# Kernel optimization log

Measured on AMD Instinct MI355X. Metric: run time of the kernel, lower is better.

The kernel has to match this reference:

```python
import jax, jax.numpy as jnp
import numpy as np

NUM_REP = 3

def setup_inputs() -> dict:
    N, E, DIM, R2, L, B, NEG = 20000, 100000, 32, 100, 4, 4, 32
    ks = jax.random.split(jax.random.key(0), 12)
    # all negatives in a row share the same head (required by the model's assert)
    h = jax.random.randint(ks[0], (B, 1), 0, N)
    t = jax.random.randint(ks[1], (B, NEG), 0, N)
    batch = jnp.stack([jnp.broadcast_to(h, (B, NEG)), t], axis=-1)  # [B,NEG,2]
    edge_index = jax.random.randint(ks[2], (2, E), 0, N)
    edge_type = jax.random.randint(ks[3], (E,), 0, R2)
    edge_attr = 0.1 * jax.random.normal(ks[4], (E, DIM), jnp.float32)
    start_query = jax.random.normal(ks[5], (NUM_REP, DIM), jnp.float32)
    W_rel = jax.random.normal(ks[6], (L, DIM, R2 * DIM), jnp.float32) * (DIM ** -0.5)
    b_rel = jnp.zeros((L, R2 * DIM), jnp.float32)
    W_lin = jax.random.normal(ks[7], (L, 2 * DIM, DIM), jnp.float32) * ((2 * DIM) ** -0.5)
    b_lin = jnp.zeros((L, DIM), jnp.float32)
    W_mlp1 = jax.random.normal(ks[8], (DIM, DIM), jnp.float32) * (DIM ** -0.5)
    b_mlp1 = jnp.zeros((DIM,), jnp.float32)
    W_mlp2 = jax.random.normal(ks[9], (DIM, DIM), jnp.float32) * (DIM ** -0.5)
    b_mlp2 = jnp.zeros((DIM,), jnp.float32)
    return {"batch": batch, "edge_index": edge_index, "edge_type": edge_type,
            "edge_attr": edge_attr, "num_nodes": N, "start_query": start_query,
            "W_rel": W_rel, "b_rel": b_rel, "W_lin": W_lin, "b_lin": b_lin,
            "W_mlp1": W_mlp1, "b_mlp1": b_mlp1, "W_mlp2": W_mlp2, "b_mlp2": b_mlp2}

def reference(batch, edge_index, edge_type, edge_attr, num_nodes, start_query,
              W_rel, b_rel, W_lin, b_lin, W_mlp1, b_mlp1, W_mlp2, b_mlp2):
    B, num_neg, _ = batch.shape
    N = int(num_nodes)
    dim = start_query.shape[1]
    L = W_rel.shape[0]
    bs = NUM_REP * B
    batch_full = jnp.tile(batch, (NUM_REP, 1, 1))            # [bs, neg, 2]
    query_idx = jnp.repeat(jnp.arange(NUM_REP), B)           # [bs]
    h_index, t_index = batch_full[..., 0], batch_full[..., 1]
    # negative_sample_to_tail (no-op when heads are constant per row, as built)
    is_t_neg = jnp.all(h_index == h_index[:, :1], axis=-1, keepdims=True)
    h_index, t_index = (jnp.where(is_t_neg, h_index, t_index),
                        jnp.where(is_t_neg, t_index, h_index))
    h0 = h_index[:, 0]
    q = start_query[query_idx]                               # [bs, dim]
    rows = jnp.arange(bs)
    boundary = jnp.zeros((bs, N, dim), q.dtype).at[rows, h0].add(q)
    pb = jnp.zeros((bs, N), q.dtype).at[rows, h0].set(1.0)   # path boundary
    src, dst = edge_index[0], edge_index[1]
    x = boundary
    for l in range(L):
        # dependent per-query relation embeddings: [bs, 2R, dim]
        rel = (q @ W_rel[l] + b_rel[l]).reshape(bs, -1, dim)
        rel_e = rel[:, edge_type] + edge_attr[None]          # [bs, E, dim]
        msg = x[:, src] * rel_e                              # distmult message
        # sum aggregation; boundary acts as the self-loop message
        agg = jnp.zeros((bs, N, dim), x.dtype).at[:, dst].add(msg) + boundary
        x = jax.nn.relu(jnp.concatenate([x, agg], axis=-1) @ W_lin[l] + b_lin[l])
        # reachability propagation of the path boundary (scatter-max)
        pb = jnp.maximum(pb, jnp.zeros((bs, N), pb.dtype).at[:, dst].max(pb[:, src]))
    feat_t = x[rows[:, None], t_index]                       # [bs, neg, dim]
    feat = feat_t.reshape(NUM_REP, B, num_neg, dim).mean(0)  # mean over reps
    features = jax.nn.relu(feat @ W_mlp1 + b_mlp1) @ W_mlp2 + b_mlp2
    pb_t = pb[rows[:, None], t_index][..., None]             # [bs, neg, 1]
    path_boundary = pb_t.reshape(NUM_REP, B, num_neg, 1).max(0)
    return features, path_boundary
```

## Files before the change

kernel.cpp:

```cpp
#include <hip/hip_runtime.h>

#define N_NODES 20000
#define N_EDGES 100000
#define DIM 32
#define R2 100
#define NLAYERS 4
#define BATCH 4
#define NEG 32
#define NREP 3
#define BS (NREP * BATCH)
#define RELDIM (R2 * DIM)

#define NPB 4
#define TPN 96
#define LBLK (NPB * TPN)
#define GRID_LAYER (N_NODES / NPB)

#define EB ((N_EDGES + 255) / 256)
#define NB ((N_NODES + 255) / 256)
#define RELB ((NLAYERS * R2 * BS * DIM) / 256)
#define PREP_GRID (EB + NB + RELB)

#define XO_A 0
#define XO_B (XO_A + (size_t)N_NODES * BS * DIM)
#define PBO_A (XO_B + (size_t)N_NODES * BS * DIM)
#define PBO_B (PBO_A + (size_t)N_NODES * BS)
#define RELO (PBO_B + (size_t)N_NODES * BS)
#define QO (RELO + (size_t)NLAYERS * R2 * BS * DIM)
#define FLOAT_TOTAL (QO + (size_t)BS * DIM)

#define IO_H0 0
#define IO_TIDX (IO_H0 + BS)
#define IO_COUNTS (IO_TIDX + BS * NEG)
#define IO_OFF (IO_COUNTS + N_NODES)
#define IO_BCUR (IO_OFF + N_NODES + 1)
#define IO_CURSOR (IO_BCUR + 256 * 32)
#define IO_ORDER (IO_CURSOR + N_NODES)
#define IO_PAD (IO_ORDER + N_NODES)
#define IO_ES (((IO_PAD + 1) / 2) * 2)
#define INT_TOTAL (IO_ES + 2 * N_EDGES)

__global__ void k_count(const int* __restrict__ dst, int* __restrict__ counts) {
    int e = blockIdx.x * blockDim.x + threadIdx.x;
    if (e < N_EDGES) atomicAdd(&counts[dst[e]], 1);
}

__global__ void k_scan(const int* __restrict__ counts, int* __restrict__ off,
                       int* __restrict__ cursor, int* __restrict__ bcursor,
                       const int* __restrict__ batch,
                       const float* __restrict__ start_query,
                       float* __restrict__ q, int* __restrict__ h0,
                       int* __restrict__ t_idx) {
    __shared__ int sd[1024];
    __shared__ int hist[256];
    int t = threadIdx.x;

    if (t < BS) {
        int r = t;
        int b = r % BATCH, rep = r / BATCH;
        int h00 = batch[(b * NEG + 0) * 2 + 0];
        bool is_t_neg = true;
        for (int j = 0; j < NEG; j++)
            if (batch[(b * NEG + j) * 2 + 0] != h00) { is_t_neg = false; break; }
        int hsel = is_t_neg ? 0 : 1;
        int h0v = batch[(b * NEG + 0) * 2 + hsel];
        h0[r] = h0v;
        for (int j = 0; j < NEG; j++)
            t_idx[r * NEG + j] = batch[(b * NEG + j) * 2 + (1 - hsel)];
        for (int d = 0; d < DIM; d++) q[r * DIM + d] = start_query[rep * DIM + d];
    }

    const int CH = (N_NODES + 1023) / 1024;
    int base = t * CH;
    for (int i = t; i < 256; i += 1024) hist[i] = 0;
    int sum = 0;
    for (int i = 0; i < CH; i++) {
        int idx = base + i;
        if (idx < N_NODES) sum += counts[idx];
    }
    sd[t] = sum;
    __syncthreads();
    for (int o = 1; o < 1024; o <<= 1) {
        int v = (t >= o) ? sd[t - o] : 0;
        __syncthreads();
        sd[t] += v;
        __syncthreads();
    }
    int excl = sd[t] - sum;
    int run = excl;
    for (int i = 0; i < CH; i++) {
        int idx = base + i;
        if (idx < N_NODES) {
            int c = counts[idx];
            off[idx] = run;
            cursor[idx] = run;
            run += c;
            atomicAdd(&hist[c < 255 ? c : 255], 1);
        }
    }
    if (t == 1023) off[N_NODES] = sd[1023];
    __syncthreads();
    if (t == 0) {
        int acc = 0;
        for (int b = 255; b >= 0; b--) { bcursor[b * 32] = acc; acc += hist[b]; }
    }
}

__global__ void k_prep(const int* __restrict__ src, const int* __restrict__ dst,
                       const int* __restrict__ etype, int* __restrict__ cursor,
                       int2* __restrict__ es,
                       const int* __restrict__ counts, int* __restrict__ bcursor,
                       int* __restrict__ node_order,
                       const float* __restrict__ q, const float* __restrict__ W_rel,
                       const float* __restrict__ b_rel, float* __restrict__ rel) {
    int bid = blockIdx.x;
    if (bid < EB) {
        int e = bid * 256 + threadIdx.x;
        if (e < N_EDGES) {
            int p = atomicAdd(&cursor[dst[e]], 1);
            es[p] = make_int2(src[e] | (etype[e] << 20), e);
        }
    } else if (bid < EB + NB) {
        int n = (bid - EB) * 256 + threadIdx.x;
        if (n < N_NODES) {
            int deg = counts[n]; if (deg > 255) deg = 255;
            int pos = atomicAdd(&bcursor[deg * 32], 1);
            node_order[pos] = n;
        }
    } else {
        int idx = (bid - EB - NB) * 256 + threadIdx.x;
        int d = idx & 31;
        int r = (idx >> 5) % BS;
        int et = (idx / (BS * DIM)) % R2;
        int l = idx / (R2 * BS * DIM);
        int c = et * DIM + d;
        const float* W = W_rel + (size_t)l * DIM * RELDIM;
        float acc = b_rel[l * RELDIM + c];
        #pragma unroll
        for (int k = 0; k < DIM; k++) acc += q[r * DIM + k] * W[(size_t)k * RELDIM + c];
        rel[idx] = acc;
    }
}

template <bool L0>
__launch_bounds__(LBLK)
__global__ void k_layer(const float* __restrict__ x_old, const float* __restrict__ pb_old,
                        const float* __restrict__ rel_l, const float* __restrict__ edge_attr,
                        const int2* __restrict__ es, const int* __restrict__ off,
                        const int* __restrict__ node_order,
                        const int* __restrict__ h0, const float* __restrict__ q,
                        const float* __restrict__ W_lin_l, const float* __restrict__ b_lin_l,
                        float* __restrict__ x_new, float* __restrict__ pb_new) {
    __shared__ float sW[64 * DIM];
    __shared__ float sB[DIM];
    __shared__ float sIn[NPB * BS * 68];
    __shared__ int sFlag;

    const int gi = threadIdx.x / TPN;
    const int t = threadIdx.x % TPN;
    const int r = t >> 3;
    const int l = t & 7;
    const int n = node_order[blockIdx.x * NPB + gi];

    const int h0r = h0[r];
    const float4 q4 = *(const float4*)(q + r * DIM + l * 4);
    const int s0 = off[n], s1 = off[n + 1];

    if (L0) {
        if (threadIdx.x == 0) sFlag = 0;
        bool spec = (n == h0r);
        for (int k = s0; k < s1; k++) {
            int2 p2 = es[k];
            if ((p2.x & 0xFFFFF) == h0r) spec = true;
        }
        __syncthreads();
        if (spec) sFlag = 1;
        __syncthreads();
        if (!sFlag) {
            float4 b4 = *(const float4*)(b_lin_l + l * 4);
            b4.x = fmaxf(b4.x, 0.f); b4.y = fmaxf(b4.y, 0.f);
            b4.z = fmaxf(b4.z, 0.f); b4.w = fmaxf(b4.w, 0.f);
            *(float4*)(x_new + ((size_t)n * BS + r) * DIM + l * 4) = b4;
            if (l == 0) pb_new[n * BS + r] = 0.f;
            return;
        }
    }

    for (int i = threadIdx.x; i < 64 * DIM; i += LBLK) sW[i] = W_lin_l[i];
    if (threadIdx.x < DIM) sB[threadIdx.x] = b_lin_l[threadIdx.x];

    float4 xr4, ag4 = make_float4(0.f, 0.f, 0.f, 0.f);
    float pbm;
    if (L0) {
        xr4 = (n == h0r) ? q4 : make_float4(0.f, 0.f, 0.f, 0.f);
        pbm = (n == h0r) ? 1.f : 0.f;
    } else {
        xr4 = *(const float4*)(x_old + ((size_t)n * BS + r) * DIM + l * 4);
        pbm = pb_old[n * BS + r];
    }

    #pragma unroll 2
    for (int k = s0; k < s1; k++) {
        int2 p2 = es[k];
        int s = p2.x & 0xFFFFF;
        int et = ((unsigned)p2.x) >> 20;
        int e = p2.y;
        if (L0) {
            if (s == h0r) {
                float4 rl = *(const float4*)(rel_l + ((size_t)et * BS + r) * DIM + l * 4);
                float4 ea = *(const float4*)(edge_attr + (size_t)e * DIM + l * 4);
                ag4.x += q4.x * (rl.x + ea.x);
                ag4.y += q4.y * (rl.y + ea.y);
                ag4.z += q4.z * (rl.z + ea.z);
                ag4.w += q4.w * (rl.w + ea.w);
                pbm = 1.f;
            }
        } else {
            float4 xs = *(const float4*)(x_old + ((size_t)s * BS + r) * DIM + l * 4);
            float4 rl = *(const float4*)(rel_l + ((size_t)et * BS + r) * DIM + l * 4);
            float4 ea = *(const float4*)(edge_attr + (size_t)e * DIM + l * 4);
            ag4.x += xs.x * (rl.x + ea.x);
            ag4.y += xs.y * (rl.y + ea.y);
            ag4.z += xs.z * (rl.z + ea.z);
            ag4.w += xs.w * (rl.w + ea.w);
            pbm = fmaxf(pbm, pb_old[s * BS + r]);
        }
    }
    if (n == h0r) {
        ag4.x += q4.x; ag4.y += q4.y; ag4.z += q4.z; ag4.w += q4.w;
    }

    float* srow = sIn + (gi * BS + r) * 68;
    *(float4*)(srow + l * 4) = xr4;
    *(float4*)(srow + 32 + l * 4) = ag4;
    __syncthreads();

    float4 acc = *(const float4*)(sB + l * 4);
    #pragma unroll
    for (int k4 = 0; k4 < 16; k4++) {
        float4 v = *(const float4*)(srow + k4 * 4);
        const float* wb = sW + (k4 * 4) * DIM + l * 4;
        float4 w0 = *(const float4*)(wb);
        float4 w1 = *(const float4*)(wb + DIM);
        float4 w2 = *(const float4*)(wb + 2 * DIM);
        float4 w3 = *(const float4*)(wb + 3 * DIM);
        acc.x += v.x * w0.x + v.y * w1.x + v.z * w2.x + v.w * w3.x;
        acc.y += v.x * w0.y + v.y * w1.y + v.z * w2.y + v.w * w3.y;
        acc.z += v.x * w0.z + v.y * w1.z + v.z * w2.z + v.w * w3.z;
        acc.w += v.x * w0.w + v.y * w1.w + v.z * w2.w + v.w * w3.w;
    }
    acc.x = fmaxf(acc.x, 0.f);
    acc.y = fmaxf(acc.y, 0.f);
    acc.z = fmaxf(acc.z, 0.f);
    acc.w = fmaxf(acc.w, 0.f);
    *(float4*)(x_new + ((size_t)n * BS + r) * DIM + l * 4) = acc;
    if (l == 0) pb_new[n * BS + r] = pbm;
}

__launch_bounds__(1024)
__global__ void k_final(const float* __restrict__ x, const float* __restrict__ pb,
                        const int* __restrict__ t_idx,
                        const float* __restrict__ W1, const float* __restrict__ b1,
                        const float* __restrict__ W2, const float* __restrict__ b2,
                        float* __restrict__ out) {
    __shared__ float sW1[DIM * DIM];
    __shared__ float sW2[DIM * DIM];
    __shared__ float sfeat[BATCH * NEG * DIM];
    __shared__ float shid[BATCH * NEG * DIM];
    const int t = threadIdx.x;
    const int NPAIR = BATCH * NEG;

    for (int i = t; i < DIM * DIM; i += 1024) { sW1[i] = W1[i]; sW2[i] = W2[i]; }

    for (int i = t; i < NPAIR * DIM; i += 1024) {
        int pair = i >> 5;
        int d = i & 31;
        int b = pair >> 5;
        int tt = t_idx[pair];
        float s = 0.f;
        #pragma unroll
        for (int rep = 0; rep < NREP; rep++)
            s += x[((size_t)tt * BS + rep * BATCH + b) * DIM + d];
        sfeat[i] = s * (1.f / 3.f);
    }
    __syncthreads();

    for (int i = t; i < NPAIR * DIM; i += 1024) {
        int pair = i >> 5;
        int jj = i & 31;
        float a = b1[jj];
        #pragma unroll
        for (int k = 0; k < DIM; k++)
            a += sfeat[pair * DIM + k] * sW1[k * DIM + jj];
        shid[i] = fmaxf(a, 0.f);
    }
    __syncthreads();

    for (int i = t; i < NPAIR * DIM; i += 1024) {
        int pair = i >> 5;
        int jj = i & 31;
        float a = b2[jj];
        #pragma unroll
        for (int k = 0; k < DIM; k++)
            a += shid[pair * DIM + k] * sW2[k * DIM + jj];
        out[i] = a;
    }

    if (t < NPAIR) {
        int b = t >> 5;
        int tt = t_idx[t];
        float pm = 0.f;
        #pragma unroll
        for (int rep = 0; rep < NREP; rep++)
            pm = fmaxf(pm, pb[(size_t)tt * BS + rep * BATCH + b]);
        out[NPAIR * DIM + t] = pm;
    }
}

extern "C" void kernel_launch(void* const* d_in, const int* in_sizes, int n_in,
                              void* d_out, int out_size, void* d_ws, size_t ws_size,
                              hipStream_t stream) {
    const int* batch = (const int*)d_in[0];
    const int* edge_index = (const int*)d_in[1];
    const int* edge_type = (const int*)d_in[2];
    const float* edge_attr = (const float*)d_in[3];
    const float* start_query = (const float*)d_in[5];
    const float* W_rel = (const float*)d_in[6];
    const float* b_rel = (const float*)d_in[7];
    const float* W_lin = (const float*)d_in[8];
    const float* b_lin = (const float*)d_in[9];
    const float* W_mlp1 = (const float*)d_in[10];
    const float* b_mlp1 = (const float*)d_in[11];
    const float* W_mlp2 = (const float*)d_in[12];
    const float* b_mlp2 = (const float*)d_in[13];

    float* wf = (float*)d_ws;
    int* wi = (int*)(wf + FLOAT_TOTAL);
    size_t need = FLOAT_TOTAL * sizeof(float) + INT_TOTAL * sizeof(int);
    if (ws_size < need) return;

    float* x_a = wf + XO_A;
    float* x_b = wf + XO_B;
    float* pb_a = wf + PBO_A;
    float* pb_b = wf + PBO_B;
    float* rel = wf + RELO;
    float* q = wf + QO;
    int* h0 = wi + IO_H0;
    int* t_idx = wi + IO_TIDX;
    int* counts = wi + IO_COUNTS;
    int* off = wi + IO_OFF;
    int* bcursor = wi + IO_BCUR;
    int* cursor = wi + IO_CURSOR;
    int* node_order = wi + IO_ORDER;
    int2* es = (int2*)(wi + IO_ES);

    const int* src = edge_index;
    const int* dst = edge_index + N_EDGES;

    hipMemsetAsync(counts, 0, (size_t)N_NODES * sizeof(int), stream);

    k_count<<<EB, 256, 0, stream>>>(dst, counts);
    k_scan<<<1, 1024, 0, stream>>>(counts, off, cursor, bcursor,
                                   batch, start_query, q, h0, t_idx);
    k_prep<<<PREP_GRID, 256, 0, stream>>>(src, dst, edge_type, cursor, es,
                                          counts, bcursor, node_order,
                                          q, W_rel, b_rel, rel);

    k_layer<true><<<GRID_LAYER, LBLK, 0, stream>>>(
        x_a, pb_a, rel, edge_attr, es, off, node_order, h0, q,
        W_lin, b_lin, x_a, pb_a);

    float* x_cur = x_a;
    float* x_nxt = x_b;
    float* pb_cur = pb_a;
    float* pb_nxt = pb_b;
    for (int l = 1; l < NLAYERS; l++) {
        k_layer<false><<<GRID_LAYER, LBLK, 0, stream>>>(
            x_cur, pb_cur, rel + (size_t)l * R2 * BS * DIM, edge_attr, es, off,
            node_order, h0, q,
            W_lin + (size_t)l * 64 * DIM, b_lin + (size_t)l * DIM,
            x_nxt, pb_nxt);
        float* tx = x_cur; x_cur = x_nxt; x_nxt = tx;
        float* tp = pb_cur; pb_cur = pb_nxt; pb_nxt = tp;
    }

    k_final<<<1, 1024, 0, stream>>>(x_cur, pb_cur, t_idx, W_mlp1, b_mlp1, W_mlp2, b_mlp2,
                                    (float*)d_out);
}
```

Baseline: 345.4 us.

## Fuse degree count and scan into one LDS kernel; trim redundant per-lane loads

Replaces the memset, the global-atomic degree-count kernel and the scan kernel with one single-block kernel. That kernel builds the degree histogram in a shared-memory array of N_NODES ints, then scans it; k_prep now derives each node's degree from the offsets. In the layer kernel, only lane l==0 of each row scans edges for the head-node check and loads path-boundary values, which removes duplicated loads across the 8 lanes. The edge-loop unroll also goes from 2 to 4. The one-block build does all edge atomics serially across 1024 threads and needs about 80KB of LDS.

Result: slower. 421.7 us (+22.1%).

```diff
diff --git a/kernel.cpp b/kernel.cpp
--- a/kernel.cpp
+++ b/kernel.cpp
@@ -31,8 +31,7 @@
 
 #define IO_H0 0
 #define IO_TIDX (IO_H0 + BS)
-#define IO_COUNTS (IO_TIDX + BS * NEG)
-#define IO_OFF (IO_COUNTS + N_NODES)
+#define IO_OFF (IO_TIDX + BS * NEG)
 #define IO_BCUR (IO_OFF + N_NODES + 1)
 #define IO_CURSOR (IO_BCUR + 256 * 32)
 #define IO_ORDER (IO_CURSOR + N_NODES)
@@ -40,20 +39,21 @@
 #define IO_ES (((IO_PAD + 1) / 2) * 2)
 #define INT_TOTAL (IO_ES + 2 * N_EDGES)
 
-__global__ void k_count(const int* __restrict__ dst, int* __restrict__ counts) {
-    int e = blockIdx.x * blockDim.x + threadIdx.x;
-    if (e < N_EDGES) atomicAdd(&counts[dst[e]], 1);
-}
-
-__global__ void k_scan(const int* __restrict__ counts, int* __restrict__ off,
-                       int* __restrict__ cursor, int* __restrict__ bcursor,
-                       const int* __restrict__ batch,
-                       const float* __restrict__ start_query,
-                       float* __restrict__ q, int* __restrict__ h0,
-                       int* __restrict__ t_idx) {
+__launch_bounds__(1024)
+__global__ void k_build(const int* __restrict__ dst,
+                        const int* __restrict__ batch,
+                        const float* __restrict__ start_query,
+                        int* __restrict__ off, int* __restrict__ cursor,
+                        int* __restrict__ bcursor,
+                        float* __restrict__ q, int* __restrict__ h0,
+                        int* __restrict__ t_idx) {
+    __shared__ int hist[N_NODES];
     __shared__ int sd[1024];
-    __shared__ int hist[256];
-    int t = threadIdx.x;
+    __shared__ int hist256[256];
+    const int t = threadIdx.x;
+
+    for (int i = t; i < N_NODES; i += 1024) hist[i] = 0;
+    for (int i = t; i < 256; i += 1024) hist256[i] = 0;
 
     if (t < BS) {
         int r = t;
@@ -69,14 +69,17 @@
             t_idx[r * NEG + j] = batch[(b * NEG + j) * 2 + (1 - hsel)];
         for (int d = 0; d < DIM; d++) q[r * DIM + d] = start_query[rep * DIM + d];
     }
+    __syncthreads();
+
+    for (int e = t; e < N_EDGES; e += 1024) atomicAdd(&hist[dst[e]], 1);
+    __syncthreads();
 
     const int CH = (N_NODES + 1023) / 1024;
     int base = t * CH;
-    for (int i = t; i < 256; i += 1024) hist[i] = 0;
     int sum = 0;
     for (int i = 0; i < CH; i++) {
         int idx = base + i;
-        if (idx < N_NODES) sum += counts[idx];
+        if (idx < N_NODES) sum += hist[idx];
     }
     sd[t] = sum;
     __syncthreads();
@@ -86,30 +89,29 @@
         sd[t] += v;
         __syncthreads();
     }
-    int excl = sd[t] - sum;
-    int run = excl;
+    int run = sd[t] - sum;
     for (int i = 0; i < CH; i++) {
         int idx = base + i;
         if (idx < N_NODES) {
-            int c = counts[idx];
+            int c = hist[idx];
             off[idx] = run;
             cursor[idx] = run;
             run += c;
-            atomicAdd(&hist[c < 255 ? c : 255], 1);
+            atomicAdd(&hist256[c < 255 ? c : 255], 1);
         }
     }
     if (t == 1023) off[N_NODES] = sd[1023];
     __syncthreads();
     if (t == 0) {
         int acc = 0;
-        for (int b = 255; b >= 0; b--) { bcursor[b * 32] = acc; acc += hist[b]; }
+        for (int b = 255; b >= 0; b--) { bcursor[b * 32] = acc; acc += hist256[b]; }
     }
 }
 
 __global__ void k_prep(const int* __restrict__ src, const int* __restrict__ dst,
                        const int* __restrict__ etype, int* __restrict__ cursor,
                        int2* __restrict__ es,
-                       const int* __restrict__ counts, int* __restrict__ bcursor,
+                       const int* __restrict__ off, int* __restrict__ bcursor,
                        int* __restrict__ node_order,
                        const float* __restrict__ q, const float* __restrict__ W_rel,
                        const float* __restrict__ b_rel, float* __restrict__ rel) {
@@ -123,7 +125,7 @@
     } else if (bid < EB + NB) {
         int n = (bid - EB) * 256 + threadIdx.x;
         if (n < N_NODES) {
-            int deg = counts[n]; if (deg > 255) deg = 255;
+            int deg = off[n + 1] - off[n]; if (deg > 255) deg = 255;
             int pos = atomicAdd(&bcursor[deg * 32], 1);
             node_order[pos] = n;
         }
@@ -169,9 +171,11 @@
     if (L0) {
         if (threadIdx.x == 0) sFlag = 0;
         bool spec = (n == h0r);
-        for (int k = s0; k < s1; k++) {
-            int2 p2 = es[k];
-            if ((p2.x & 0xFFFFF) == h0r) spec = true;
+        if (l == 0) {
+            for (int k = s0; k < s1; k++) {
+                int2 p2 = es[k];
+                if ((p2.x & 0xFFFFF) == h0r) spec = true;
+            }
         }
         __syncthreads();
         if (spec) sFlag = 1;
@@ -196,10 +200,10 @@
         pbm = (n == h0r) ? 1.f : 0.f;
     } else {
         xr4 = *(const float4*)(x_old + ((size_t)n * BS + r) * DIM + l * 4);
-        pbm = pb_old[n * BS + r];
-    }
-
-    #pragma unroll 2
+        pbm = (l == 0) ? pb_old[n * BS + r] : 0.f;
+    }
+
+    #pragma unroll 4
     for (int k = s0; k < s1; k++) {
         int2 p2 = es[k];
         int s = p2.x & 0xFFFFF;
@@ -223,7 +227,7 @@
             ag4.y += xs.y * (rl.y + ea.y);
             ag4.z += xs.z * (rl.z + ea.z);
             ag4.w += xs.w * (rl.w + ea.w);
-            pbm = fmaxf(pbm, pb_old[s * BS + r]);
+            if (l == 0) pbm = fmaxf(pbm, pb_old[s * BS + r]);
         }
     }
     if (n == h0r) {
@@ -347,7 +351,6 @@
     float* q = wf + QO;
     int* h0 = wi + IO_H0;
     int* t_idx = wi + IO_TIDX;
-    int* counts = wi + IO_COUNTS;
     int* off = wi + IO_OFF;
     int* bcursor = wi + IO_BCUR;
     int* cursor = wi + IO_CURSOR;
@@ -357,13 +360,10 @@
     const int* src = edge_index;
     const int* dst = edge_index + N_EDGES;
 
-    hipMemsetAsync(counts, 0, (size_t)N_NODES * sizeof(int), stream);
-
-    k_count<<<EB, 256, 0, stream>>>(dst, counts);
-    k_scan<<<1, 1024, 0, stream>>>(counts, off, cursor, bcursor,
-                                   batch, start_query, q, h0, t_idx);
+    k_build<<<1, 1024, 0, stream>>>(dst, batch, start_query,
+                                    off, cursor, bcursor, q, h0, t_idx);
     k_prep<<<PREP_GRID, 256, 0, stream>>>(src, dst, edge_type, cursor, es,
-                                          counts, bcursor, node_order,
+                                          off, bcursor, node_order,
                                           q, W_rel, b_rel, rel);
 
     k_layer<true><<<GRID_LAYER, LBLK, 0, stream>>>(
```
